# Kernel optimization log

Measured on AMD Instinct MI355X. Metric: run time of the kernel, lower is better.

Reference implementation:

```python
import jax, jax.numpy as jnp
import numpy as np

IN_DIM = 256
OUT_DIM = 64
NUM_HEADS = 4
N = 6144


def setup_inputs() -> dict:
    key = jax.random.key(0)
    ks = jax.random.split(key, 9)
    h = jax.random.normal(ks[0], (N, IN_DIM), dtype=jnp.float32)
    # dense multiplicative adjacency weights, one [N,N] matrix per head
    adj = jax.random.uniform(ks[1], (NUM_HEADS, N, N), dtype=jnp.float32)
    s = 1.0 / np.sqrt(IN_DIM)
    WQ = jax.random.normal(ks[2], (NUM_HEADS, IN_DIM, OUT_DIM), dtype=jnp.float32) * s
    WK = jax.random.normal(ks[3], (NUM_HEADS, IN_DIM, OUT_DIM), dtype=jnp.float32) * s
    WV = jax.random.normal(ks[4], (NUM_HEADS, IN_DIM, OUT_DIM), dtype=jnp.float32) * s
    bQ = jax.random.normal(ks[5], (NUM_HEADS, OUT_DIM), dtype=jnp.float32) * 0.01
    bK = jax.random.normal(ks[6], (NUM_HEADS, OUT_DIM), dtype=jnp.float32) * 0.01
    bV = jax.random.normal(ks[7], (NUM_HEADS, OUT_DIM), dtype=jnp.float32) * 0.01
    return {"adj": adj, "h": h, "WQ": WQ, "bQ": bQ, "WK": WK, "bK": bK, "WV": WV, "bV": bV}


def reference(adj, h, WQ, bQ, WK, bK, WV, bV):
    # Per-head projections, batched over heads: [H, N, out_dim]
    Qh = jnp.einsum('nd,hdo->hno', h, WQ) + bQ[:, None, :]
    Kh = jnp.einsum('nd,hdo->hno', h, WK) + bK[:, None, :]
    Vh = jnp.einsum('nd,hdo->hno', h, WV) + bV[:, None, :]
    scale = 1.0 / jnp.sqrt(jnp.asarray(h.shape[1], dtype=h.dtype))
    # multiplicative adjacency mask (NOT additive) applied before softmax
    A_tilde = scale * jnp.einsum('hno,hmo->hnm', Qh, Kh) * adj  # [H, N, N]
    attention = jax.nn.softmax(A_tilde, axis=-1)
    X = jnp.einsum('hnm,hmo->hno', attention, Vh)  # [H, N, out_dim]
    return X
```

## Files before the change

### kernel.cpp

```cpp
#include <hip/hip_runtime.h>
#include <hip/hip_bf16.h>

#define NN 6144
#define HEADS 4
#define DIN 256
#define DOUT 64

typedef __bf16 bf16_t;
typedef bf16_t bf16x8 __attribute__((ext_vector_type(8)));
typedef float f32x16 __attribute__((ext_vector_type(16)));
typedef float f32x4 __attribute__((ext_vector_type(4)));
typedef unsigned u32x4 __attribute__((ext_vector_type(4)));

#if __has_builtin(__builtin_amdgcn_exp2f)
#define EXP2(x) __builtin_amdgcn_exp2f(x)
#else
#define EXP2(x) exp2f(x)
#endif

static __device__ __forceinline__ f32x16 zero16() {
  f32x16 z;
#pragma unroll
  for (int i = 0; i < 16; ++i) z[i] = 0.0f;
  return z;
}

static __device__ __forceinline__ bf16x8 ldg8(const bf16_t* p) {
  return *reinterpret_cast<const bf16x8*>(p);
}

static __device__ __forceinline__ unsigned pk2(float a, float b) {
  union { bf16_t h[2]; unsigned u; } z;
  z.h[0] = (bf16_t)a;
  z.h[1] = (bf16_t)b;
  return z.u;
}

static __device__ __forceinline__ void pswap(unsigned& x, unsigned& y) {
  asm("v_permlane32_swap_b32 %0, %1" : "+v"(x), "+v"(y));
}

static __device__ __forceinline__ f32x4 ldnt4(const float* p) {
  return __builtin_nontemporal_load(reinterpret_cast<const f32x4*>(p));
}

#define SCHED0() __builtin_amdgcn_sched_barrier(0)
#define VW(N)                                                   \
  asm volatile("s_waitcnt vmcnt(" #N ")" ::: "memory");         \
  SCHED0();

__global__ __launch_bounds__(256) void prep_kernel(
    const float* __restrict__ h, const float* __restrict__ WQ,
    const float* __restrict__ WK, const float* __restrict__ WV,
    bf16_t* __restrict__ hb, bf16_t* __restrict__ Wt) {
  int stride = gridDim.x * blockDim.x;
  int idx = blockIdx.x * blockDim.x + threadIdx.x;
  for (int i = idx; i < NN * DIN; i += stride)
    hb[i] = (bf16_t)h[i];
  const float c2 = 0.0625f * 1.4426950408889634f;
  for (int i = idx; i < 3 * HEADS * DOUT * DIN; i += stride) {
    int d = i & (DIN - 1);
    int o = (i >> 8) & (DOUT - 1);
    int hh = (i >> 14) & (HEADS - 1);
    int m = i >> 16;
    const float* W = (m == 0) ? WQ : (m == 1) ? WK : WV;
    float v = W[(hh * DIN + d) * DOUT + o];
    if (m == 0) v *= c2;
    Wt[i] = (bf16_t)v;
  }
}

__global__ __launch_bounds__(256) void proj_kernel(
    const bf16_t* __restrict__ hb, const bf16_t* __restrict__ Wt,
    const float* __restrict__ bQ, const float* __restrict__ bK,
    const float* __restrict__ bV,
    bf16_t* __restrict__ Qb, bf16_t* __restrict__ Kf, bf16_t* __restrict__ Vf) {
  const float c2 = 0.0625f * 1.4426950408889634f;
  int tid = threadIdx.x;
  int w = tid >> 6, l = tid & 63;
  int l31 = l & 31, lh = l >> 5;
  int hh = blockIdx.y;
  int n0 = blockIdx.x * 64;

#pragma unroll
  for (int s = 0; s < 3; ++s) {
    int t = w * 3 + s;
    if (t < 8) {
      int m = t >> 2;
      int rh = (t >> 1) & 1;
      int oh = t & 1;
      const bf16_t* arow = hb + (n0 + rh * 32 + l31) * DIN + 8 * lh;
      const bf16_t* brow = Wt + ((m * HEADS + hh) * DOUT + oh * 32 + l31) * DIN + 8 * lh;
      f32x16 acc = zero16();
#pragma unroll
      for (int kc = 0; kc < 16; ++kc)
        acc = __builtin_amdgcn_mfma_f32_32x32x16_bf16(ldg8(arow + kc * 16),
                                                      ldg8(brow + kc * 16), acc, 0, 0, 0);
      const float* bias = (m == 0) ? bQ : bK;
      float bv = bias[hh * DOUT + oh * 32 + l31];
      if (m == 0) {
        bv *= c2;
        bf16_t* outp = Qb + (size_t)(hh * NN + n0 + rh * 32) * DOUT + oh * 32 + l31;
#pragma unroll
        for (int r = 0; r < 16; ++r) {
          int q = (r & 3) + 8 * (r >> 2) + 4 * lh;
          outp[q * DOUT] = (bf16_t)(acc[r] + bv);
        }
      } else {
        int o = oh * 32 + l31;
        bf16_t* outp = Kf + (size_t)hh * 393216 + (n0 >> 6) * 4096 + rh * 2048 +
                       (o >> 4) * 512 + ((o >> 3) & 1) * 256 + (o & 7);
#pragma unroll
        for (int r = 0; r < 16; ++r) {
          int rr = (r & 3) + 8 * (r >> 2) + 4 * lh;
          outp[rr * 8] = (bf16_t)(acc[r] + bv);
        }
      }
    } else {
      int tt = t - 8;
      int oh = tt >> 1, nh = tt & 1;
      const bf16_t* arow = Wt + ((2 * HEADS + hh) * DOUT + oh * 32 + l31) * DIN + 8 * lh;
      const bf16_t* brow = hb + (n0 + nh * 32 + l31) * DIN + 8 * lh;
      f32x16 acc = zero16();
#pragma unroll
      for (int kc = 0; kc < 16; ++kc)
        acc = __builtin_amdgcn_mfma_f32_32x32x16_bf16(ldg8(arow + kc * 16),
                                                      ldg8(brow + kc * 16), acc, 0, 0, 0);
      int k6 = nh * 32 + l31;
      bf16_t* outp = Vf + (size_t)hh * 393216 + (n0 >> 6) * 4096 + oh * 2048 +
                     (k6 >> 4) * 512 + ((k6 >> 3) & 1) * 256 + (k6 & 7);
#pragma unroll
      for (int r = 0; r < 16; ++r) {
        int rr = (r & 3) + 8 * (r >> 2) + 4 * lh;
        float bvv = bV[hh * DOUT + oh * 32 + rr];
        outp[rr * 8] = (bf16_t)(acc[r] + bvv);
      }
    }
  }
}

#define ATTN_BODY(AIN, AOUT, IT, CUR)                                          \
  {                                                                            \
    int tc = t0 + (IT);                                                        \
    if (tc >= 24) tc -= 24;                                                    \
    int tni = t0 + (IT) + 2;                                                   \
    if (tni >= 24) tni -= 24;                                                  \
    int chunk = tc * 4 + w;                                                    \
    const bf16_t* kbase = Kh + (size_t)chunk * 4096 + l * 8;                   \
    const bf16_t* vbase = Vh + (size_t)chunk * 4096 + l * 8;                   \
    bf16x8 kf[8], vf[8];                                                       \
    _Pragma("unroll") for (int x = 0; x < 4; ++x) {                            \
      kf[x] = ldg8(kbase + x * 512);                                           \
      kf[4 + x] = ldg8(kbase + 2048 + x * 512);                                \
    }                                                                          \
    _Pragma("unroll") for (int x = 0; x < 4; ++x) {                            \
      vf[x] = ldg8(vbase + x * 512);                                           \
      vf[4 + x] = ldg8(vbase + 2048 + x * 512);                                \
    }                                                                          \
    SCHED0();                                                                  \
    if ((IT) < 22) {      \
      _Pragma("unroll") for (int i = 0; i < 8; ++i) {                          \
        int row = 8 * w + i;                                                   \
        AOUT[i] = ldnt4(adjq + (size_t)row * NN + tni * 256 + ((l ^ i) << 2)); \
      }                                                                        \
    }                                                                          \
    SCHED0();                                                                  \
    f32x4 av[8];                                                               \
    _Pragma("unroll") for (int t2 = 0; t2 < 2; ++t2)                           \
        _Pragma("unroll") for (int g = 0; g < 4; ++g) {                        \
      int c = 16 * w + 8 * t2 + 2 * g + lh;                                    \
      av[t2 * 4 + g] = *reinterpret_cast<const f32x4*>(                        \
          &smem[CUR][l31][(c ^ (l31 & 7)) << 2]);                              \
    }                                                                          \
    f32x16 s0 = zero16(), s1 = zero16();                                       \
    _Pragma("unroll") for (int kc = 0; kc < 4; ++kc) {                         \
      s0 = __builtin_amdgcn_mfma_f32_32x32x16_bf16(kf[kc], qf[kc], s0, 0, 0, 0);\
      s1 = __builtin_amdgcn_mfma_f32_32x32x16_bf16(kf[4 + kc], qf[kc], s1, 0, 0, 0);\
    }                                                                          \
    _Pragma("unroll") for (int t2 = 0; t2 < 2; ++t2) {                         \
      f32x16 st = t2 ? s1 : s0;                                                \
      float p[16];                                                             \
      _Pragma("unroll") for (int r = 0; r < 16; ++r) {                         \
        float pv = EXP2(st[r] * av[4 * t2 + (r >> 2)][r & 3]);                 \
        p[r] = pv;                                                             \
        sacc += pv;                                                            \
      }                                                                        \
      _Pragma("unroll") for (int c2 = 0; c2 < 2; ++c2) {                       \
        unsigned wA0 = pk2(p[8 * c2 + 0], p[8 * c2 + 1]);                      \
        unsigned wB0 = pk2(p[8 * c2 + 2], p[8 * c2 + 3]);                      \
        unsigned wA1 = pk2(p[8 * c2 + 4], p[8 * c2 + 5]);                      \
        unsigned wB1 = pk2(p[8 * c2 + 6], p[8 * c2 + 7]);                      \
        pswap(wA0, wA1);                                                       \
        pswap(wB0, wB1);                                                       \
        u32x4 pw;                                                              \
        pw[0] = wA0; pw[1] = wB0; pw[2] = wA1; pw[3] = wB1;                    \
        bf16x8 pb = __builtin_bit_cast(bf16x8, pw);                            \
        int kc = 2 * t2 + c2;                                                  \
        o0 = __builtin_amdgcn_mfma_f32_32x32x16_bf16(vf[kc], pb, o0, 0, 0, 0); \
        o1 = __builtin_amdgcn_mfma_f32_32x32x16_bf16(vf[4 + kc], pb, o1, 0, 0, 0);\
      }                                                                        \
    }                                                                          \
    if ((IT) < 23) {          \
      VW(8)                                                                    \
      _Pragma("unroll") for (int i = 0; i < 8; ++i) {                          \
        int row = 8 * w + i;                                                   \
        *reinterpret_cast<f32x4*>(&smem[(CUR) ^ 1][row][l << 2]) = AIN[i];     \
      }                                                                        \
      asm volatile("s_waitcnt lgkmcnt(0)" ::: "memory");                       \
      SCHED0();                                                                \
      __builtin_amdgcn_s_barrier();                                           \
      SCHED0();                                                                \
    }                                                                          \
  }

__global__ __launch_bounds__(256, 2) void attn_kernel(
    const float* __restrict__ adj, const bf16_t* __restrict__ Qb,
    const bf16_t* __restrict__ Kf, const bf16_t* __restrict__ Vf,
    float* __restrict__ out) {
  __shared__ __align__(16) float smem[2][32][256];

  int tid = threadIdx.x;
  int w = tid >> 6, l = tid & 63;
  int l31 = l & 31, lh = l >> 5;

  int bid = blockIdx.x;
  int work = (bid & 7) * 96 + (bid >> 3);
  int hh = work / 192;
  int q0 = (work % 192) * 32;
  int t0 = bid % 24;

  const bf16_t* Qrow = Qb + (size_t)(hh * NN + q0 + l31) * DOUT + 8 * lh;
  bf16x8 qf[4];
#pragma unroll
  for (int kc = 0; kc < 4; ++kc) qf[kc] = ldg8(Qrow + kc * 16);

  const bf16_t* Kh = Kf + (size_t)hh * 393216;
  const bf16_t* Vh = Vf + (size_t)hh * 393216;
  const float* adjq = adj + (size_t)hh * NN * NN + (size_t)q0 * NN;

  f32x16 o0 = zero16(), o1 = zero16();
  float sacc = 0.0f;

  f32x4 aregA[8], aregB[8];

#pragma unroll
  for (int i = 0; i < 8; ++i) {
    int row = 8 * w + i;
    aregA[i] = ldnt4(adjq + (size_t)row * NN + t0 * 256 + ((l ^ i) << 2));
  }
  int t1 = t0 + 1;
  if (t1 >= 24) t1 -= 24;
#pragma unroll
  for (int i = 0; i < 8; ++i) {
    int row = 8 * w + i;
    aregB[i] = ldnt4(adjq + (size_t)row * NN + t1 * 256 + ((l ^ i) << 2));
  }
  VW(8)
#pragma unroll
  for (int i = 0; i < 8; ++i) {
    int row = 8 * w + i;
    *reinterpret_cast<f32x4*>(&smem[0][row][l << 2]) = aregA[i];
  }
  asm volatile("s_waitcnt lgkmcnt(0)" ::: "memory");
  SCHED0();
  __builtin_amdgcn_s_barrier();
  SCHED0();

  for (int it2 = 0; it2 < 12; ++it2) {
    ATTN_BODY(aregB, aregA, 2 * it2, 0)
    ATTN_BODY(aregA, aregB, 2 * it2 + 1, 1)
  }

  VW(0)
  __syncthreads();

  float stot = sacc + __shfl_xor(sacc, 32);
  float* opart = &smem[0][0][0];
  float* ssum = &smem[0][0][0] + 8192;
  if (l < 32) ssum[w * 32 + l31] = stot;
#pragma unroll
  for (int r = 0; r < 16; ++r) {
    int d = (r & 3) + 8 * (r >> 2) + 4 * lh;
    opart[w * 2048 + d * 32 + l31] = o0[r];
    opart[w * 2048 + (32 + d) * 32 + l31] = o1[r];
  }
  __syncthreads();

#pragma unroll
  for (int k = 0; k < 8; ++k) {
    int idx = k * 256 + tid;
    int q = idx & 31, d = idx >> 5;
    float s = ssum[q] + ssum[32 + q] + ssum[64 + q] + ssum[96 + q];
    float ov = opart[d * 32 + q] + opart[2048 + d * 32 + q] +
               opart[4096 + d * 32 + q] + opart[6144 + d * 32 + q];
    out[(size_t)(hh * NN + q0 + q) * DOUT + d] = ov / s;
  }
}

extern "C" void kernel_launch(void* const* d_in, const int* in_sizes, int n_in,
                              void* d_out, int out_size, void* d_ws, size_t ws_size,
                              hipStream_t stream) {
  const float* adj = (const float*)d_in[0];
  const float* h   = (const float*)d_in[1];
  const float* WQ  = (const float*)d_in[2];
  const float* bQ  = (const float*)d_in[3];
  const float* WK  = (const float*)d_in[4];
  const float* bK  = (const float*)d_in[5];
  const float* WV  = (const float*)d_in[6];
  const float* bV  = (const float*)d_in[7];
  float* out = (float*)d_out;

  if (ws_size < 12976128) return;

  char* ws = (char*)d_ws;
  bf16_t* hb = (bf16_t*)ws;
  bf16_t* Wt = (bf16_t*)(ws + 3145728);
  bf16_t* Qb = (bf16_t*)(ws + 3538944);
  bf16_t* Kf = (bf16_t*)(ws + 6684672);
  bf16_t* Vf = (bf16_t*)(ws + 9830400);

  prep_kernel<<<1024, 256, 0, stream>>>(h, WQ, WK, WV, hb, Wt);
  proj_kernel<<<dim3(96, 4), 256, 0, stream>>>(hb, Wt, bQ, bK, bV, Qb, Kf, Vf);
  attn_kernel<<<768, 256, 0, stream>>>(adj, Qb, Kf, Vf, out);
}
```

Measured before the change: 160.9 us.

## Split attention key range across two blocks with atomic accumulation and normalize pass

Splits each (head, query-tile) attention work item into two halves along the key dimension, doubling the grid to 1536 blocks. Partial outputs and softmax denominators are combined with atomicAdd into zero-initialized buffers, and a new normalization kernel divides by the summed denominator. The aim is better occupancy and load balance across CUs on a memory-bound kernel, at the cost of output zeroing, atomics, and an extra kernel launch. The LDS reduction layout is also padded to stride 33 to avoid bank conflicts.

```diff
diff --git a/kernel.cpp b/kernel.cpp
--- a/kernel.cpp
+++ b/kernel.cpp
@@ -52,11 +52,13 @@
 __global__ __launch_bounds__(256) void prep_kernel(
     const float* __restrict__ h, const float* __restrict__ WQ,
     const float* __restrict__ WK, const float* __restrict__ WV,
-    bf16_t* __restrict__ hb, bf16_t* __restrict__ Wt) {
+    bf16_t* __restrict__ hb, bf16_t* __restrict__ Wt,
+    float* __restrict__ out, float* __restrict__ denom) {
   int stride = gridDim.x * blockDim.x;
   int idx = blockIdx.x * blockDim.x + threadIdx.x;
-  for (int i = idx; i < NN * DIN; i += stride)
-    hb[i] = (bf16_t)h[i];
+  for (int i = idx; i < HEADS * NN * DOUT; i += stride) out[i] = 0.0f;
+  for (int i = idx; i < HEADS * NN; i += stride) denom[i] = 0.0f;
+  for (int i = idx; i < NN * DIN; i += stride) hb[i] = (bf16_t)h[i];
   const float c2 = 0.0625f * 1.4426950408889634f;
   for (int i = idx; i < 3 * HEADS * DOUT * DIN; i += stride) {
     int d = i & (DIN - 1);
@@ -142,10 +144,11 @@
 #define ATTN_BODY(AIN, AOUT, IT, CUR)                                          \
   {                                                                            \
     int tc = t0 + (IT);                                                        \
-    if (tc >= 24) tc -= 24;                                                    \
+    if (tc >= 12) tc -= 12;                                                    \
     int tni = t0 + (IT) + 2;                                                   \
-    if (tni >= 24) tni -= 24;                                                  \
-    int chunk = tc * 4 + w;                                                    \
+    if (tni >= 12) tni -= 12;                                                  \
+    if (tni >= 12) tni -= 12;                                                  \
+    int chunk = ckb + tc * 4 + w;                                              \
     const bf16_t* kbase = Kh + (size_t)chunk * 4096 + l * 8;                   \
     const bf16_t* vbase = Vh + (size_t)chunk * 4096 + l * 8;                   \
     bf16x8 kf[8], vf[8];                                                       \
@@ -158,7 +161,7 @@
       vf[4 + x] = ldg8(vbase + 2048 + x * 512);                                \
     }                                                                          \
     SCHED0();                                                                  \
-    if ((IT) < 22) {      \
+    if ((IT) < 10) {                                      \
       _Pragma("unroll") for (int i = 0; i < 8; ++i) {                          \
         int row = 8 * w + i;                                                   \
         AOUT[i] = ldnt4(adjq + (size_t)row * NN + tni * 256 + ((l ^ i) << 2)); \
@@ -200,7 +203,7 @@
         o1 = __builtin_amdgcn_mfma_f32_32x32x16_bf16(vf[4 + kc], pb, o1, 0, 0, 0);\
       }                                                                        \
     }                                                                          \
-    if ((IT) < 23) {          \
+    if ((IT) < 11) {          \
       VW(8)                                                                    \
       _Pragma("unroll") for (int i = 0; i < 8; ++i) {                          \
         int row = 8 * w + i;                                                   \
@@ -216,7 +219,7 @@
 __global__ __launch_bounds__(256, 2) void attn_kernel(
     const float* __restrict__ adj, const bf16_t* __restrict__ Qb,
     const bf16_t* __restrict__ Kf, const bf16_t* __restrict__ Vf,
-    float* __restrict__ out) {
+    float* __restrict__ out, float* __restrict__ denom) {
   __shared__ __align__(16) float smem[2][32][256];
 
   int tid = threadIdx.x;
@@ -224,10 +227,13 @@
   int l31 = l & 31, lh = l >> 5;
 
   int bid = blockIdx.x;
-  int work = (bid & 7) * 96 + (bid >> 3);
-  int hh = work / 192;
-  int q0 = (work % 192) * 32;
-  int t0 = bid % 24;
+  int x = bid & 7;
+  int hh = x >> 1;
+  int ky = x & 1;
+  int qt = bid >> 3;
+  int q0 = qt * 32;
+  int t0 = qt % 12;
+  const int ckb = ky * 48;
 
   const bf16_t* Qrow = Qb + (size_t)(hh * NN + q0 + l31) * DOUT + 8 * lh;
   bf16x8 qf[4];
@@ -236,7 +242,7 @@
 
   const bf16_t* Kh = Kf + (size_t)hh * 393216;
   const bf16_t* Vh = Vf + (size_t)hh * 393216;
-  const float* adjq = adj + (size_t)hh * NN * NN + (size_t)q0 * NN;
+  const float* adjq = adj + (size_t)hh * NN * NN + (size_t)q0 * NN + ky * 3072;
 
   f32x16 o0 = zero16(), o1 = zero16();
   float sacc = 0.0f;
@@ -249,7 +255,7 @@
     aregA[i] = ldnt4(adjq + (size_t)row * NN + t0 * 256 + ((l ^ i) << 2));
   }
   int t1 = t0 + 1;
-  if (t1 >= 24) t1 -= 24;
+  if (t1 >= 12) t1 -= 12;
 #pragma unroll
   for (int i = 0; i < 8; ++i) {
     int row = 8 * w + i;
@@ -266,7 +272,7 @@
   __builtin_amdgcn_s_barrier();
   SCHED0();
 
-  for (int it2 = 0; it2 < 12; ++it2) {
+  for (int it2 = 0; it2 < 6; ++it2) {
     ATTN_BODY(aregB, aregA, 2 * it2, 0)
     ATTN_BODY(aregA, aregB, 2 * it2 + 1, 1)
   }
@@ -276,25 +282,38 @@
 
   float stot = sacc + __shfl_xor(sacc, 32);
   float* opart = &smem[0][0][0];
-  float* ssum = &smem[0][0][0] + 8192;
+  float* ssum = opart + 4 * 64 * 33;
   if (l < 32) ssum[w * 32 + l31] = stot;
 #pragma unroll
   for (int r = 0; r < 16; ++r) {
     int d = (r & 3) + 8 * (r >> 2) + 4 * lh;
-    opart[w * 2048 + d * 32 + l31] = o0[r];
-    opart[w * 2048 + (32 + d) * 32 + l31] = o1[r];
+    opart[w * 2112 + d * 33 + l31] = o0[r];
+    opart[w * 2112 + (32 + d) * 33 + l31] = o1[r];
   }
   __syncthreads();
 
+  if (tid < 32)
+    atomicAdd(&denom[hh * NN + q0 + tid],
+              ssum[tid] + ssum[32 + tid] + ssum[64 + tid] + ssum[96 + tid]);
 #pragma unroll
   for (int k = 0; k < 8; ++k) {
     int idx = k * 256 + tid;
-    int q = idx & 31, d = idx >> 5;
-    float s = ssum[q] + ssum[32 + q] + ssum[64 + q] + ssum[96 + q];
-    float ov = opart[d * 32 + q] + opart[2048 + d * 32 + q] +
-               opart[4096 + d * 32 + q] + opart[6144 + d * 32 + q];
-    out[(size_t)(hh * NN + q0 + q) * DOUT + d] = ov / s;
-  }
+    int d = idx & 63, q = idx >> 6;
+    float ov = opart[d * 33 + q] + opart[2112 + d * 33 + q] +
+               opart[4224 + d * 33 + q] + opart[6336 + d * 33 + q];
+    atomicAdd(&out[(size_t)(hh * NN + q0 + q) * DOUT + d], ov);
+  }
+}
+
+__global__ __launch_bounds__(256) void norm_kernel(
+    float* __restrict__ out, const float* __restrict__ denom) {
+  int i = blockIdx.x * 256 + threadIdx.x;
+  float dn = denom[i >> 4];
+  f32x4 v = reinterpret_cast<f32x4*>(out)[i];
+  float inv = 1.0f / dn;
+#pragma unroll
+  for (int j = 0; j < 4; ++j) v[j] *= inv;
+  reinterpret_cast<f32x4*>(out)[i] = v;
 }
 
 extern "C" void kernel_launch(void* const* d_in, const int* in_sizes, int n_in,
@@ -310,16 +329,18 @@
   const float* bV  = (const float*)d_in[7];
   float* out = (float*)d_out;
 
-  if (ws_size < 12976128) return;
+  if (ws_size < 13074432) return;
 
   char* ws = (char*)d_ws;
-  bf16_t* hb = (bf16_t*)ws;
-  bf16_t* Wt = (bf16_t*)(ws + 3145728);
-  bf16_t* Qb = (bf16_t*)(ws + 3538944);
-  bf16_t* Kf = (bf16_t*)(ws + 6684672);
-  bf16_t* Vf = (bf16_t*)(ws + 9830400);
-
-  prep_kernel<<<1024, 256, 0, stream>>>(h, WQ, WK, WV, hb, Wt);
+  bf16_t* hb    = (bf16_t*)ws;
+  bf16_t* Wt    = (bf16_t*)(ws + 3145728);
+  bf16_t* Qb    = (bf16_t*)(ws + 3538944);
+  bf16_t* Kf    = (bf16_t*)(ws + 6684672);
+  bf16_t* Vf    = (bf16_t*)(ws + 9830400);
+  float*  denom = (float*)(ws + 12976128);
+
+  prep_kernel<<<1024, 256, 0, stream>>>(h, WQ, WK, WV, hb, Wt, out, denom);
   proj_kernel<<<dim3(96, 4), 256, 0, stream>>>(hb, Wt, bQ, bK, bV, Qb, Kf, Vf);
-  attn_kernel<<<768, 256, 0, stream>>>(adj, Qb, Kf, Vf, out);
-}
+  attn_kernel<<<1536, 256, 0, stream>>>(adj, Qb, Kf, Vf, out, denom);
+  norm_kernel<<<1536, 256, 0, stream>>>(out, denom);
+}
```

After: 159.8 us. About the same (-0.7%).
